# Kernel optimization log

Measured on AMD Instinct MI355X. Metric: run time of the kernel, lower is better.

## Reference

```python
import jax, jax.numpy as jnp
import numpy as np

MARGIN = 0.3
EPS = 1e-6  # torch TripletMarginLoss pairwise_distance eps


def setup_inputs() -> dict:
    key = jax.random.key(0)
    k1, k2 = jax.random.split(key)
    n, d = 8192, 128
    inputs = jax.random.normal(k1, (n, d), dtype=jnp.float32)
    similarity = jax.random.randint(k2, (n, n), 0, 2, dtype=jnp.int32)
    return {"inputs": inputs, "similarity": similarity}


def reference(inputs, similarity):
    # mask[i, j] = True if j is a positive of anchor i
    mask = similarity != 0                      # (n, n) bool
    maskf = mask.astype(inputs.dtype)
    counts = maskf.sum(axis=1, keepdims=True)   # (n, 1), >0 by construction
    # per-anchor center = mean of its positives (masked mean as a GEMM)
    centers = (maskf @ inputs) / counts         # (n, d)
    # dist[i, j] = ||centers[i] - inputs[j]||_2 via the expansion trick
    # (avoids materializing the (n, n, d) difference tensor of the original)
    c2 = jnp.sum(centers * centers, axis=1)[:, None]
    x2 = jnp.sum(inputs * inputs, axis=1)[None, :]
    d2 = c2 + x2 - 2.0 * (centers @ inputs.T)
    dist = jnp.sqrt(jnp.maximum(d2, 0.0))       # (n, n)
    # dist only feeds argmin in the original (indices carry no grad)
    dist = jax.lax.stop_gradient(dist)
    # hard-negative mining: argmin of dist over negatives of each anchor
    neg_idx = jnp.argmin(jnp.where(mask, jnp.inf, dist), axis=1)  # (n,)
    neg_min = inputs[neg_idx]                   # (n, d)
    # TripletMarginLoss(margin=0.3, p=2): anchor=centers, pos=inputs, neg=neg_min
    d_ap = jnp.linalg.norm(centers - inputs + EPS, axis=1)
    d_an = jnp.linalg.norm(centers - neg_min + EPS, axis=1)
    return jnp.mean(jnp.maximum(d_ap - d_an + MARGIN, 0.0))
```

## Files before the change

### kernel.cpp

```cpp
#include <hip/hip_runtime.h>
#include <stdint.h>

#define NN 8192
#define DD 128

typedef float f32x4 __attribute__((ext_vector_type(4)));
typedef short bf16x8 __attribute__((ext_vector_type(8)));

union B8 { uint32_t u[4]; bf16x8 v; };

__device__ inline uint16_t f2bf(float f) {
  uint32_t u = __builtin_bit_cast(uint32_t, f);
  uint32_t r = (u + 0x7FFFu + ((u >> 16) & 1u)) >> 16;
  return (uint16_t)r;
}

__device__ inline f32x4 mfma16(bf16x8 a, bf16x8 b, f32x4 c) {
  return __builtin_amdgcn_mfma_f32_16x16x32_bf16(a, b, c, 0, 0, 0);
}

__global__ __launch_bounds__(256) void k_prep(const float* __restrict__ inp,
                                              uint16_t* __restrict__ inp_bf,
                                              uint16_t* __restrict__ inpT_bf,
                                              float* __restrict__ x2p,
                                              uint32_t* __restrict__ counts,
                                              uint32_t* __restrict__ negkey,
                                              float* __restrict__ out) {
  __shared__ uint16_t ldsT[128 * 65];
  __shared__ float ldsS[256];
  const int tid = threadIdx.x;
  const int gid = blockIdx.x * 256 + tid;
  if (gid < NN) { counts[gid] = 0u; negkey[gid] = 0xFFFFFFFFu; }
  if (gid == 0) out[0] = 0.f;
  const int j0 = blockIdx.x * 64;
  const int r = tid >> 2;
  const int dseg = (tid & 3) * 32;
  float ss = 0.f;
#pragma unroll
  for (int it = 0; it < 8; ++it) {
    float4 v = *(const float4*)(inp + (size_t)(j0 + r) * DD + dseg + it * 4);
    ss += v.x * v.x + v.y * v.y + v.z * v.z + v.w * v.w;
    uint16_t b0 = f2bf(v.x), b1 = f2bf(v.y), b2 = f2bf(v.z), b3 = f2bf(v.w);
    *(ushort4*)(inp_bf + (size_t)(j0 + r) * DD + dseg + it * 4) = make_ushort4(b0, b1, b2, b3);
    int d = dseg + it * 4;
    ldsT[(d + 0) * 65 + r] = b0;
    ldsT[(d + 1) * 65 + r] = b1;
    ldsT[(d + 2) * 65 + r] = b2;
    ldsT[(d + 3) * 65 + r] = b3;
  }
  ldsS[tid] = ss;
  __syncthreads();
  if (tid < 64)
    x2p[j0 + tid] = ldsS[tid * 4] + ldsS[tid * 4 + 1] + ldsS[tid * 4 + 2] + ldsS[tid * 4 + 3] + 512.0f;
#pragma unroll
  for (int it = 0; it < 32; ++it) {
    int flat = it * 256 + tid;
    int d = flat >> 6, jl = flat & 63;
    inpT_bf[(size_t)d * NN + j0 + jl] = ldsT[d * 65 + jl];
  }
}

__global__ __launch_bounds__(256, 4) void k_maskmm(const int* __restrict__ sim,
                                                   const uint16_t* __restrict__ inpT,
                                                   uint32_t* __restrict__ bmT,
                                                   uint32_t* __restrict__ counts,
                                                   float* __restrict__ part) {
  __shared__ __align__(16) uint16_t ldsB[128 * 40];
  __shared__ uint32_t ldsM[64];
  __shared__ uint32_t ldsW[32 * 64];
  const int tid = threadIdx.x, lane = tid & 63, w = tid >> 6;
  const int col = lane & 15, quad = lane >> 4;
  const int m0 = blockIdx.x * 64;
  const int kb0 = blockIdx.y * 1024;
  const int wm = (w >> 1) * 32, wn = (w & 1) * 64;
  const int dim = tid >> 1, koff = (tid & 1) * 16;
  const int rbase = w * 16 + (lane >> 5);
  const int scol = lane & 31;

  f32x4 acc[2][4];
  const f32x4 z = {0.f, 0.f, 0.f, 0.f};
#pragma unroll
  for (int r = 0; r < 2; ++r)
#pragma unroll
    for (int c = 0; c < 4; ++c) acc[r][c] = z;

  bf16x8 bpf0 = *(const bf16x8*)(inpT + (size_t)dim * NN + kb0 + koff);
  bf16x8 bpf1 = *(const bf16x8*)(inpT + (size_t)dim * NN + kb0 + koff + 8);
  int sv[8];
#pragma unroll
  for (int i = 0; i < 8; ++i)
    sv[i] = sim[(size_t)(m0 + rbase + 2 * i) * NN + kb0 + scol];
  uint32_t cnt[8];
#pragma unroll
  for (int i = 0; i < 8; ++i) cnt[i] = 0u;

  for (int ks = 0; ks < 32; ++ks) {
    const int kb = kb0 + ks * 32;
    __syncthreads();
    *(bf16x8*)(ldsB + dim * 40 + koff) = bpf0;
    *(bf16x8*)(ldsB + dim * 40 + koff + 8) = bpf1;
#pragma unroll
    for (int i = 0; i < 8; ++i) {
      unsigned long long ball = __ballot(sv[i] != 0);
      uint32_t word = (uint32_t)(ball >> (lane & 32));
      if ((lane & 31) == 0) {
        int rr = rbase + 2 * i;
        ldsM[rr] = word;
        ldsW[ks * 64 + rr] = word;
        cnt[i] += (uint32_t)__popc(word);
      }
    }
    __syncthreads();
    if (ks < 31) {
      bpf0 = *(const bf16x8*)(inpT + (size_t)dim * NN + kb + 32 + koff);
      bpf1 = *(const bf16x8*)(inpT + (size_t)dim * NN + kb + 32 + koff + 8);
#pragma unroll
      for (int i = 0; i < 8; ++i)
        sv[i] = sim[(size_t)(m0 + rbase + 2 * i) * NN + kb + 32 + scol];
    }
    B8 af[2];
#pragma unroll
    for (int rr = 0; rr < 2; ++rr) {
      uint32_t word = ldsM[wm + rr * 16 + col];
      uint32_t b = (word >> (quad * 8)) & 0xFFu;
      uint32_t s = b * 0x8001u;
#pragma unroll
      for (int p = 0; p < 4; ++p) {
        uint32_t t = (s >> (2 * p)) & 0x10001u;
        af[rr].u[p] = t * 0x3F80u;
      }
    }
#pragma unroll
    for (int cc = 0; cc < 4; ++cc) {
      bf16x8 bfr = *(const bf16x8*)(ldsB + (wn + cc * 16 + col) * 40 + quad * 8);
#pragma unroll
      for (int rr = 0; rr < 2; ++rr) acc[rr][cc] = mfma16(af[rr].v, bfr, acc[rr][cc]);
    }
  }
  if ((lane & 31) == 0) {
#pragma unroll
    for (int i = 0; i < 8; ++i)
      atomicAdd(&counts[m0 + rbase + 2 * i], cnt[i]);
  }
  float* pp = part + (size_t)blockIdx.y * NN * DD;
#pragma unroll
  for (int rr = 0; rr < 2; ++rr)
#pragma unroll
    for (int cc = 0; cc < 4; ++cc)
#pragma unroll
      for (int g = 0; g < 4; ++g)
        pp[(size_t)(m0 + wm + rr * 16 + quad * 4 + g) * DD + wn + cc * 16 + col] = acc[rr][cc][g];
  __syncthreads();
#pragma unroll
  for (int it = 0; it < 8; ++it) {
    int idx = it * 256 + tid;
    int kw = idx >> 6, r = idx & 63;
    bmT[(size_t)((kb0 >> 5) + kw) * NN + m0 + r] = ldsW[idx];
  }
}

__global__ __launch_bounds__(256) void k_reduce(const float* __restrict__ part,
                                                const uint32_t* __restrict__ counts,
                                                float* __restrict__ centers,
                                                uint16_t* __restrict__ cen_bf) {
  const int gid = blockIdx.x * 256 + threadIdx.x;
  const int idx = gid * 4;
  const int row = idx >> 7;
  const float inv = 1.0f / (float)counts[row];
  float4 v = *(const float4*)(part + idx);
#pragma unroll
  for (int s = 1; s < 8; ++s) {
    float4 u = *(const float4*)(part + (size_t)s * NN * DD + idx);
    v.x += u.x; v.y += u.y; v.z += u.z; v.w += u.w;
  }
  v.x *= inv; v.y *= inv; v.z *= inv; v.w *= inv;
  *(float4*)(centers + idx) = v;
  *(ushort4*)(cen_bf + idx) = make_ushort4(f2bf(v.x), f2bf(v.y), f2bf(v.z), f2bf(v.w));
}

__global__ __launch_bounds__(256, 4) void k_argmin(const uint16_t* __restrict__ cen_bf,
                                                   const uint16_t* __restrict__ inp_bf,
                                                   const uint32_t* __restrict__ bmT,
                                                   const float* __restrict__ x2p,
                                                   uint32_t* __restrict__ negkey) {
  __shared__ __align__(16) uint16_t ldsB[64 * 136];
  __shared__ uint32_t ldsM[128];
  __shared__ float ldsX[64];
  __shared__ uint32_t ldsR[64];
  const int tid = threadIdx.x, lane = tid & 63, w = tid >> 6;
  const int col = lane & 15, quad = lane >> 4;
  const int i0 = blockIdx.x * 64;
  const int jbase = blockIdx.y * 1024;
  const int wi = (w >> 1) * 32, wj = (w & 1) * 32;
  bf16x8 af[2][4];
#pragma unroll
  for (int rr = 0; rr < 2; ++rr)
#pragma unroll
    for (int kk = 0; kk < 4; ++kk)
      af[rr][kk] = *(const bf16x8*)(cen_bf + (size_t)(i0 + wi + rr * 16 + col) * DD + kk * 32 + quad * 8);
  if (tid < 64) ldsR[tid] = 0xFFFFFFFFu;
  uint32_t best[2][4];
#pragma unroll
  for (int rr = 0; rr < 2; ++rr)
#pragma unroll
    for (int g = 0; g < 4; ++g) best[rr][g] = 0xFFFFFFFFu;

  const int jl = tid >> 2, doff = (tid & 3) * 32;
  bf16x8 bpf[4];
#pragma unroll
  for (int it = 0; it < 4; ++it)
    bpf[it] = *(const bf16x8*)(inp_bf + (size_t)(jbase + jl) * DD + doff + it * 8);
  uint32_t mpf = (tid < 128) ? bmT[(size_t)((jbase >> 5) + (tid >> 6)) * NN + i0 + (tid & 63)] : 0u;
  float xpf = (tid >= 128 && tid < 192) ? x2p[jbase + tid - 128] : 0.f;

  for (int js = 0; js < 16; ++js) {
    const int j0 = jbase + js * 64;
    __syncthreads();
#pragma unroll
    for (int it = 0; it < 4; ++it)
      *(bf16x8*)(ldsB + jl * 136 + doff + it * 8) = bpf[it];
    if (tid < 128) ldsM[tid] = mpf;
    else if (tid < 192) ldsX[tid - 128] = xpf;
    __syncthreads();
    if (js < 15) {
#pragma unroll
      for (int it = 0; it < 4; ++it)
        bpf[it] = *(const bf16x8*)(inp_bf + (size_t)(j0 + 64 + jl) * DD + doff + it * 8);
      if (tid < 128) mpf = bmT[(size_t)(((j0 + 64) >> 5) + (tid >> 6)) * NN + i0 + (tid & 63)];
      else if (tid < 192) xpf = x2p[j0 + 64 + tid - 128];
    }
    f32x4 acc[2][2];
    const f32x4 z = {0.f, 0.f, 0.f, 0.f};
    acc[0][0] = z; acc[0][1] = z; acc[1][0] = z; acc[1][1] = z;
#pragma unroll
    for (int kk = 0; kk < 4; ++kk) {
      bf16x8 b0 = *(const bf16x8*)(ldsB + (wj + col) * 136 + kk * 32 + quad * 8);
      bf16x8 b1 = *(const bf16x8*)(ldsB + (wj + 16 + col) * 136 + kk * 32 + quad * 8);
      acc[0][0] = mfma16(af[0][kk], b0, acc[0][0]);
      acc[0][1] = mfma16(af[0][kk], b1, acc[0][1]);
      acc[1][0] = mfma16(af[1][kk], b0, acc[1][0]);
      acc[1][1] = mfma16(af[1][kk], b1, acc[1][1]);
    }
    const uint32_t wsel = (w & 1) * 64;
    uint32_t words[2][4];
#pragma unroll
    for (int rr = 0; rr < 2; ++rr)
#pragma unroll
      for (int g = 0; g < 4; ++g) words[rr][g] = ldsM[wsel + wi + rr * 16 + quad * 4 + g];
#pragma unroll
    for (int cc = 0; cc < 2; ++cc) {
      const int jj = wj + cc * 16 + col;
      const float xq = ldsX[jj];
      const uint32_t jpre = (uint32_t)(j0 + jj);
      const int sh = 31 - (cc * 16 + col);
#pragma unroll
      for (int rr = 0; rr < 2; ++rr)
#pragma unroll
        for (int g = 0; g < 4; ++g) {
          float v = fmaf(-2.0f, acc[rr][cc][g], xq);
          uint32_t u = __builtin_bit_cast(uint32_t, v);
          uint32_t key = (u & 0xFFFFE000u) | jpre;
          key |= (words[rr][g] << sh) & 0x80000000u;
          best[rr][g] = min(best[rr][g], key);
        }
    }
  }
#pragma unroll
  for (int rr = 0; rr < 2; ++rr)
#pragma unroll
    for (int g = 0; g < 4; ++g) {
      uint32_t k = best[rr][g];
#pragma unroll
      for (int d = 1; d < 16; d <<= 1) {
        uint32_t o = (uint32_t)__shfl_xor((int)k, d);
        k = min(k, o);
      }
      if (col == 0) atomicMin(&ldsR[wi + rr * 16 + quad * 4 + g], k);
    }
  __syncthreads();
  if (tid < 64) atomicMin(&negkey[i0 + tid], ldsR[tid]);
}

__global__ __launch_bounds__(256) void k_loss(const float* __restrict__ centers,
                                              const float* __restrict__ inp,
                                              const uint32_t* __restrict__ negkey,
                                              float* __restrict__ out) {
  __shared__ float lds[4];
  const int tid = threadIdx.x, lane = tid & 63, w = tid >> 6;
  float local = 0.f;
#pragma unroll 1
  for (int a = 0; a < 4; ++a) {
    int i = blockIdx.x * 16 + w * 4 + a;
    float2 c = *(const float2*)(centers + (size_t)i * DD + lane * 2);
    float2 x = *(const float2*)(inp + (size_t)i * DD + lane * 2);
    uint32_t ni = negkey[i] & (NN - 1);
    float2 gv = *(const float2*)(inp + (size_t)ni * DD + lane * 2);
    float e0 = c.x - x.x + 1e-6f, e1 = c.y - x.y + 1e-6f;
    float f0 = c.x - gv.x + 1e-6f, f1 = c.y - gv.y + 1e-6f;
    float dap = e0 * e0 + e1 * e1;
    float dan = f0 * f0 + f1 * f1;
#pragma unroll
    for (int d = 32; d; d >>= 1) {
      dap += __shfl_down(dap, d);
      dan += __shfl_down(dan, d);
    }
    if (lane == 0) local += fmaxf(sqrtf(dap) - sqrtf(dan) + 0.3f, 0.f);
  }
  if (lane == 0) lds[w] = local;
  __syncthreads();
  if (tid == 0) atomicAdd(out, (lds[0] + lds[1] + lds[2] + lds[3]) * (1.0f / 8192.0f));
}

extern "C" void kernel_launch(void* const* d_in, const int* in_sizes, int n_in,
                              void* d_out, int out_size, void* d_ws, size_t ws_size,
                              hipStream_t stream) {
  (void)in_sizes; (void)n_in; (void)out_size; (void)ws_size;
  const float* inp = (const float*)d_in[0];
  const int* sim = (const int*)d_in[1];
  float* out = (float*)d_out;
  char* ws = (char*)d_ws;

  uint32_t* bmT     = (uint32_t*)ws;
  float* part       = (float*)(ws + (8u << 20));
  float* centers    = (float*)(ws + (40u << 20));
  uint16_t* inp_bf  = (uint16_t*)(ws + (44u << 20));
  uint16_t* inpT_bf = (uint16_t*)(ws + (46u << 20));
  uint16_t* cen_bf  = (uint16_t*)(ws + (48u << 20));
  float* x2p        = (float*)(ws + (50u << 20));
  uint32_t* counts  = (uint32_t*)(ws + (50u << 20) + 32768u);
  uint32_t* negkey  = (uint32_t*)(ws + (50u << 20) + 65536u);

  k_prep<<<128, 256, 0, stream>>>(inp, inp_bf, inpT_bf, x2p, counts, negkey, out);
  k_maskmm<<<dim3(128, 8), 256, 0, stream>>>(sim, inpT_bf, bmT, counts, part);
  k_reduce<<<1024, 256, 0, stream>>>(part, counts, centers, cen_bf);
  k_argmin<<<dim3(128, 8), 256, 0, stream>>>(cen_bf, inp_bf, bmT, x2p, negkey);
  k_loss<<<512, 256, 0, stream>>>(centers, inp, negkey, out);
}
```

Before: 469.0 us.

## Drop LDS staging in mask GEMM; load similarity rows and B directly per lane

The masked-mean GEMM kernel now has each lane read 8 contiguous similarity ints from its own row as int4 vectors and pack them into mask bits with shuffles. Before, a ballot ran over strided column loads. The B operand is now loaded straight from global/L2 for each MFMA instead of being staged through shared memory, and each wave owns 16 rows by 128 columns. This removes all __syncthreads and the LDS traffic, and bmT words are written directly. The cost is redundant global reads of inpT across waves and no software prefetch, so the loop becomes more latency-bound.

```diff
diff --git a/kernel.cpp b/kernel.cpp
--- a/kernel.cpp
+++ b/kernel.cpp
@@ -65,98 +65,57 @@
                                                    uint32_t* __restrict__ bmT,
                                                    uint32_t* __restrict__ counts,
                                                    float* __restrict__ part) {
-  __shared__ __align__(16) uint16_t ldsB[128 * 40];
-  __shared__ uint32_t ldsM[64];
-  __shared__ uint32_t ldsW[32 * 64];
   const int tid = threadIdx.x, lane = tid & 63, w = tid >> 6;
   const int col = lane & 15, quad = lane >> 4;
   const int m0 = blockIdx.x * 64;
   const int kb0 = blockIdx.y * 1024;
-  const int wm = (w >> 1) * 32, wn = (w & 1) * 64;
-  const int dim = tid >> 1, koff = (tid & 1) * 16;
-  const int rbase = w * 16 + (lane >> 5);
-  const int scol = lane & 31;
-
-  f32x4 acc[2][4];
+  const int wrow = w * 16;
+  const int row = m0 + wrow + col;
+  const int kq = quad * 8;
+
+  f32x4 acc[8];
   const f32x4 z = {0.f, 0.f, 0.f, 0.f};
 #pragma unroll
-  for (int r = 0; r < 2; ++r)
-#pragma unroll
-    for (int c = 0; c < 4; ++c) acc[r][c] = z;
-
-  bf16x8 bpf0 = *(const bf16x8*)(inpT + (size_t)dim * NN + kb0 + koff);
-  bf16x8 bpf1 = *(const bf16x8*)(inpT + (size_t)dim * NN + kb0 + koff + 8);
-  int sv[8];
-#pragma unroll
-  for (int i = 0; i < 8; ++i)
-    sv[i] = sim[(size_t)(m0 + rbase + 2 * i) * NN + kb0 + scol];
-  uint32_t cnt[8];
-#pragma unroll
-  for (int i = 0; i < 8; ++i) cnt[i] = 0u;
+  for (int c = 0; c < 8; ++c) acc[c] = z;
+  uint32_t cnt = 0;
+
+  const int* simr = sim + (size_t)row * NN;
 
   for (int ks = 0; ks < 32; ++ks) {
     const int kb = kb0 + ks * 32;
-    __syncthreads();
-    *(bf16x8*)(ldsB + dim * 40 + koff) = bpf0;
-    *(bf16x8*)(ldsB + dim * 40 + koff + 8) = bpf1;
-#pragma unroll
-    for (int i = 0; i < 8; ++i) {
-      unsigned long long ball = __ballot(sv[i] != 0);
-      uint32_t word = (uint32_t)(ball >> (lane & 32));
-      if ((lane & 31) == 0) {
-        int rr = rbase + 2 * i;
-        ldsM[rr] = word;
-        ldsW[ks * 64 + rr] = word;
-        cnt[i] += (uint32_t)__popc(word);
-      }
-    }
-    __syncthreads();
-    if (ks < 31) {
-      bpf0 = *(const bf16x8*)(inpT + (size_t)dim * NN + kb + 32 + koff);
-      bpf1 = *(const bf16x8*)(inpT + (size_t)dim * NN + kb + 32 + koff + 8);
-#pragma unroll
-      for (int i = 0; i < 8; ++i)
-        sv[i] = sim[(size_t)(m0 + rbase + 2 * i) * NN + kb + 32 + scol];
-    }
-    B8 af[2];
-#pragma unroll
-    for (int rr = 0; rr < 2; ++rr) {
-      uint32_t word = ldsM[wm + rr * 16 + col];
-      uint32_t b = (word >> (quad * 8)) & 0xFFu;
-      uint32_t s = b * 0x8001u;
-#pragma unroll
-      for (int p = 0; p < 4; ++p) {
-        uint32_t t = (s >> (2 * p)) & 0x10001u;
-        af[rr].u[p] = t * 0x3F80u;
-      }
-    }
-#pragma unroll
-    for (int cc = 0; cc < 4; ++cc) {
-      bf16x8 bfr = *(const bf16x8*)(ldsB + (wn + cc * 16 + col) * 40 + quad * 8);
-#pragma unroll
-      for (int rr = 0; rr < 2; ++rr) acc[rr][cc] = mfma16(af[rr].v, bfr, acc[rr][cc]);
-    }
-  }
-  if ((lane & 31) == 0) {
-#pragma unroll
-    for (int i = 0; i < 8; ++i)
-      atomicAdd(&counts[m0 + rbase + 2 * i], cnt[i]);
-  }
+    int4 s0 = *(const int4*)(simr + kb + kq);
+    int4 s1 = *(const int4*)(simr + kb + kq + 4);
+    uint32_t b = (uint32_t)s0.x | ((uint32_t)s0.y << 1) | ((uint32_t)s0.z << 2) |
+                 ((uint32_t)s0.w << 3) | ((uint32_t)s1.x << 4) | ((uint32_t)s1.y << 5) |
+                 ((uint32_t)s1.z << 6) | ((uint32_t)s1.w << 7);
+    uint32_t t = (uint32_t)__shfl_xor((int)b, 16);
+    uint32_t p2 = (quad & 1) ? ((b << 8) | t) : ((t << 8) | b);
+    uint32_t u2 = (uint32_t)__shfl_xor((int)p2, 32);
+    uint32_t word = (quad < 2) ? (p2 | (u2 << 16)) : (u2 | (p2 << 16));
+    if (quad == 0) {
+      cnt += (uint32_t)__popc(word);
+      bmT[(size_t)(kb >> 5) * NN + row] = word;
+    }
+    B8 af;
+    uint32_t s = b * 0x8001u;
+#pragma unroll
+    for (int p = 0; p < 4; ++p) {
+      uint32_t t2 = (s >> (2 * p)) & 0x10001u;
+      af.u[p] = t2 * 0x3F80u;
+    }
+#pragma unroll
+    for (int cc = 0; cc < 8; ++cc) {
+      bf16x8 bfr = *(const bf16x8*)(inpT + (size_t)(cc * 16 + col) * NN + kb + kq);
+      acc[cc] = mfma16(af.v, bfr, acc[cc]);
+    }
+  }
+  if (quad == 0) atomicAdd(&counts[row], cnt);
   float* pp = part + (size_t)blockIdx.y * NN * DD;
 #pragma unroll
-  for (int rr = 0; rr < 2; ++rr)
-#pragma unroll
-    for (int cc = 0; cc < 4; ++cc)
-#pragma unroll
-      for (int g = 0; g < 4; ++g)
-        pp[(size_t)(m0 + wm + rr * 16 + quad * 4 + g) * DD + wn + cc * 16 + col] = acc[rr][cc][g];
-  __syncthreads();
-#pragma unroll
-  for (int it = 0; it < 8; ++it) {
-    int idx = it * 256 + tid;
-    int kw = idx >> 6, r = idx & 63;
-    bmT[(size_t)((kb0 >> 5) + kw) * NN + m0 + r] = ldsW[idx];
-  }
+  for (int cc = 0; cc < 8; ++cc)
+#pragma unroll
+    for (int g = 0; g < 4; ++g)
+      pp[(size_t)(m0 + wrow + quad * 4 + g) * DD + cc * 16 + col] = acc[cc][g];
 }
 
 __global__ __launch_bounds__(256) void k_reduce(const float* __restrict__ part,
```

After: 522.6 us. 11.4% more time.
